# Kernel optimization log

Measured on AMD Instinct MI355X. Metric: run time of the kernel, lower is better.

The kernel has to match this reference:

```python
import jax, jax.numpy as jnp
import numpy as np

B, S, D, H = 4, 2048, 768, 12
DK = D // H


def setup_inputs() -> dict:
    key = jax.random.key(0)
    ks = jax.random.split(key, 12)
    s = 1.0 / np.sqrt(D)
    return {
        "query": jax.random.normal(ks[0], (B, S, D), jnp.float32),
        "key_": jax.random.normal(ks[1], (B, S, D), jnp.float32),
        "value": jax.random.normal(ks[2], (B, S, D), jnp.float32),
        "mask": jax.random.randint(ks[3], (B, S), 0, 2, jnp.int32),
        # nn.Linear weights are (out_features, in_features); y = x @ W.T + b
        "Wq": jax.random.normal(ks[4], (D, D), jnp.float32) * s,
        "bq": jnp.zeros((D,), jnp.float32),
        "Wk": jax.random.normal(ks[5], (D, D), jnp.float32) * s,
        "bk": jnp.zeros((D,), jnp.float32),
        "Wv": jax.random.normal(ks[6], (D, D), jnp.float32) * s,
        "bv": jnp.zeros((D,), jnp.float32),
        "Wo": jax.random.normal(ks[7], (D, D), jnp.float32) * s,
        "bo": jnp.zeros((D,), jnp.float32),
    }


def reference(query, key_, value, mask, Wq, bq, Wk, bk, Wv, bv, Wo, bo):
    b = query.shape[0]
    # QKV projections, split heads: (B, S, D) -> (B, H, S, DK)
    def proj(x, W, bia):
        y = x @ W.T + bia
        return y.reshape(b, -1, H, DK).transpose(0, 2, 1, 3)

    q = proj(query, Wq, bq)
    k = proj(key_, Wk, bk)
    v = proj(value, Wv, bv)

    # Scaled dot-product attention with full [B, H, S, S] score matrix
    scores = jnp.einsum("bhqd,bhkd->bhqk", q, k) / jnp.sqrt(jnp.float32(DK))
    # mask: (B, S) broadcast over heads and query positions; masked_fill(mask==0, -1e9)
    scores = jnp.where(mask[:, None, None, :] == 0, jnp.float32(-1e9), scores)
    attn = jax.nn.softmax(scores, axis=-1)
    x = jnp.einsum("bhqk,bhkd->bhqd", attn, v)  # (B, H, S, DK)

    # merge heads and output projection
    x = x.transpose(0, 2, 1, 3).reshape(b, -1, H * DK)
    return x @ Wo.T + bo
```

## Files before the change

kernel.cpp:

```cpp
#include <hip/hip_runtime.h>
#include <math.h>

#define B_  4
#define S_  2048
#define D_  768
#define H_  12
#define DK_ 64
#define M_  (B_ * S_)
#define NBH_ (B_ * H_)

typedef float f32x4 __attribute__((ext_vector_type(4)));
typedef float f32x16 __attribute__((ext_vector_type(16)));
typedef __bf16 bf16x8 __attribute__((ext_vector_type(8)));
typedef unsigned u32x4v __attribute__((ext_vector_type(4)));

#if __has_builtin(__builtin_amdgcn_exp2f)
#define EXP2(x) __builtin_amdgcn_exp2f(x)
#else
#define EXP2(x) exp2f(x)
#endif

static __device__ __forceinline__ unsigned short f2bf(float f) {
    unsigned u = __builtin_bit_cast(unsigned, f);
    u += 0x7fffu + ((u >> 16) & 1u);
    return (unsigned short)(u >> 16);
}

static __device__ __forceinline__ unsigned cvt_pk_bf16(float lo, float hi) {
    unsigned r;
    asm("v_cvt_pk_bf16_f32 %0, %1, %2" : "=v"(r) : "v"(lo), "v"(hi));
    return r;
}

static __device__ __forceinline__ void gload_lds16(const void* g, void* l) {
    __builtin_amdgcn_global_load_lds(
        (const __attribute__((address_space(1))) void*)g,
        (__attribute__((address_space(3))) void*)l, 16, 0, 0);
}

__global__ __launch_bounds__(256) void cvt_x(
    const float* __restrict__ q, const float* __restrict__ k,
    const float* __restrict__ v,
    unsigned short* __restrict__ q16, unsigned short* __restrict__ k16,
    unsigned short* __restrict__ v16)
{
    const int z = blockIdx.y;
    const float* src = (z == 0) ? q : (z == 1) ? k : v;
    unsigned short* dst = (z == 0) ? q16 : (z == 1) ? k16 : v16;
    const int NG = M_ * 96;
    for (int g = blockIdx.x * 256 + threadIdx.x; g < NG; g += gridDim.x * 256) {
        int r = g / 96, c8 = g - r * 96;
        int kt = c8 >> 2, sl = c8 & 3;
        const float* sp = src + (size_t)r * D_ + kt * 32 + sl * 8;
        float4 a = *(const float4*)sp;
        float4 b = *(const float4*)(sp + 4);
        u32x4v o;
        o.x = cvt_pk_bf16(a.x, a.y); o.y = cvt_pk_bf16(a.z, a.w);
        o.z = cvt_pk_bf16(b.x, b.y); o.w = cvt_pk_bf16(b.z, b.w);
        *(u32x4v*)(dst + (size_t)r * D_ + kt * 32 + ((sl ^ (r & 3)) << 3)) = o;
    }
}

__global__ __launch_bounds__(256) void cvt_w(
    const float* __restrict__ wq, const float* __restrict__ wk,
    const float* __restrict__ wv,
    unsigned short* __restrict__ wq16, unsigned short* __restrict__ wk16,
    unsigned short* __restrict__ wv16)
{
    const int z = blockIdx.y;
    const float* src = (z == 0) ? wq : (z == 1) ? wk : wv;
    unsigned short* dst = (z == 0) ? wq16 : (z == 1) ? wk16 : wv16;
    const int NG = D_ * 96;
    for (int g = blockIdx.x * 256 + threadIdx.x; g < NG; g += gridDim.x * 256) {
        int r = g / 96, c8 = g - r * 96;
        int kt = c8 >> 2, sl = c8 & 3;
        const float* sp = src + (size_t)r * D_ + kt * 32 + sl * 8;
        float4 a = *(const float4*)sp;
        float4 b = *(const float4*)(sp + 4);
        u32x4v o;
        o.x = cvt_pk_bf16(a.x, a.y); o.y = cvt_pk_bf16(a.z, a.w);
        o.z = cvt_pk_bf16(b.x, b.y); o.w = cvt_pk_bf16(b.z, b.w);
        *(u32x4v*)(dst + (size_t)r * D_ + kt * 32 + ((sl ^ (r & 3)) << 3)) = o;
    }
}

static __device__ __forceinline__ void gemm_body_dma(
    const unsigned short* __restrict__ A16, const unsigned short* __restrict__ B16,
    const float* __restrict__ bias, void* __restrict__ outp, const int mode,
    const float oscale)
{
    __shared__ __align__(16) unsigned short As[2][128 * 32];
    __shared__ __align__(16) unsigned short Bs[2][128 * 32];

    const int t  = threadIdx.x;
    const int l  = t & 63;
    const int w  = t >> 6;
    const int lr = l & 15;
    const int lg = l >> 4;
    const int wm = w >> 1;
    const int wn = w & 1;
    const int m0 = blockIdx.x * 128;
    const int n0 = blockIdx.y * 128;

    const unsigned short* adma = A16 + (size_t)(m0 + 32 * w + (l >> 2)) * D_ + (l & 3) * 8;
    const unsigned short* bdma = B16 + (size_t)(n0 + 32 * w + (l >> 2)) * D_ + (l & 3) * 8;

#define GSTAGE(K0, NB) do { \
        gload_lds16(adma + (K0),           &As[NB][(32 * w) * 32]); \
        gload_lds16(adma + (K0) + 16 * D_, &As[NB][(32 * w + 16) * 32]); \
        gload_lds16(bdma + (K0),           &Bs[NB][(32 * w) * 32]); \
        gload_lds16(bdma + (K0) + 16 * D_, &Bs[NB][(32 * w + 16) * 32]); \
    } while (0)

    f32x4 acc[4][4];
#pragma unroll
    for (int mi = 0; mi < 4; mi++)
#pragma unroll
        for (int ni = 0; ni < 4; ni++) acc[mi][ni] = (f32x4){0.f, 0.f, 0.f, 0.f};

    const int fsw = lr & 3;

    GSTAGE(0, 0);
    __syncthreads();

    for (int kt = 0; kt < 24; kt++) {
        const int cur = kt & 1;
        if (kt < 23) {
            if (cur) GSTAGE((kt + 1) * 32, 0);
            else     GSTAGE((kt + 1) * 32, 1);
        }

        bf16x8 af[4], bfr[4];
#pragma unroll
        for (int mi = 0; mi < 4; mi++) {
            int row = wm * 64 + mi * 16 + lr;
            af[mi] = *(const bf16x8*)&As[cur][row * 32 + ((lg ^ fsw) << 3)];
        }
#pragma unroll
        for (int ni = 0; ni < 4; ni++) {
            int row = wn * 64 + ni * 16 + lr;
            bfr[ni] = *(const bf16x8*)&Bs[cur][row * 32 + ((lg ^ fsw) << 3)];
        }
#pragma unroll
        for (int mi = 0; mi < 4; mi++)
#pragma unroll
            for (int ni = 0; ni < 4; ni++)
                acc[mi][ni] = __builtin_amdgcn_mfma_f32_16x16x32_bf16(
                    af[mi], bfr[ni], acc[mi][ni], 0, 0, 0);

        __syncthreads();
    }
#undef GSTAGE

    const int mrow0 = m0 + wm * 64;
    const int ncol0 = n0 + wn * 64;
    if (mode == 2) {
        unsigned short* out = (unsigned short*)outp;
#pragma unroll
        for (int mi = 0; mi < 4; mi++)
#pragma unroll
            for (int ni = 0; ni < 4; ni++) {
                int n = ncol0 + ni * 16 + lr;
                int h = n >> 6, dk = n & 63;
                float bv = bias[n];
                int m = mrow0 + mi * 16 + 4 * lg;
                int b = m >> 11, s = m & (S_ - 1);
                int slotp = ((s >> 3) & 7) ^ (dk & 7);
                int ssw = (s & ~63) | (slotp << 3) | (s & 7);
                uint2 o;
                o.x = cvt_pk_bf16(acc[mi][ni][0] + bv, acc[mi][ni][1] + bv);
                o.y = cvt_pk_bf16(acc[mi][ni][2] + bv, acc[mi][ni][3] + bv);
                *(uint2*)&out[((size_t)(b * H_ + h) * DK_ + dk) * S_ + ssw] = o;
            }
    } else {
        unsigned short* out = (unsigned short*)outp;
#pragma unroll
        for (int mi = 0; mi < 4; mi++)
#pragma unroll
            for (int ni = 0; ni < 4; ni++) {
                int n = ncol0 + ni * 16 + lr;
                int h = n >> 6, dk = n & 63;
                float bv = bias[n];
#pragma unroll
                for (int j = 0; j < 4; j++) {
                    int m = mrow0 + mi * 16 + 4 * lg + j;
                    int b = m >> 11, s = m & (S_ - 1);
                    int dko = (mode == 3)
                        ? ((dk & 7) | ((((dk >> 3) ^ (s & 7))) << 3)) : dk;
                    out[((size_t)(b * H_ + h) * S_ + s) * DK_ + dko] =
                        f2bf((acc[mi][ni][j] + bv) * oscale);
                }
            }
    }
}

__global__ __launch_bounds__(256) void gemm_qkv(
    const unsigned short* __restrict__ q16, const unsigned short* __restrict__ k16,
    const unsigned short* __restrict__ v16,
    const unsigned short* __restrict__ wq16, const unsigned short* __restrict__ wk16,
    const unsigned short* __restrict__ wv16,
    const float* __restrict__ bq, const float* __restrict__ bk,
    const float* __restrict__ bv,
    unsigned short* __restrict__ Qb, unsigned short* __restrict__ Kb,
    unsigned short* __restrict__ VT)
{
    const int z = blockIdx.z;
    const unsigned short* A = (z == 0) ? q16 : (z == 1) ? k16 : v16;
    const unsigned short* W = (z == 0) ? wq16 : (z == 1) ? wk16 : wv16;
    const float* bias = (z == 0) ? bq : (z == 1) ? bk : bv;
    void* out = (z == 0) ? (void*)Qb : (z == 1) ? (void*)Kb : (void*)VT;
    const int mode = (z == 0) ? 0 : (z == 1) ? 3 : 2;
    const float osc = (z == 0) ? 0.18033688011112042f : 1.0f;
    gemm_body_dma(A, W, bias, out, mode, osc);
}

__global__ __launch_bounds__(256) void proj_mfma(
    const float* __restrict__ X, const float* __restrict__ W,
    const float* __restrict__ bias, float* __restrict__ out)
{
    __shared__ __align__(16) unsigned short As[2][128 * 32];
    __shared__ __align__(16) unsigned short Bs[2][128 * 32];

    const int t  = threadIdx.x;
    const int l  = t & 63;
    const int w  = t >> 6;
    const int lr = l & 15;
    const int lg = l >> 4;
    const int wm = w >> 1;
    const int wn = w & 1;
    const int m0 = blockIdx.x * 128;
    const int n0 = blockIdx.y * 128;

    const int v0r = t >> 2,         v0s = t & 3;
    const int v1r = (t + 256) >> 2, v1s = (t + 256) & 3;
    const int off0 = v0r * 32 + ((v0s ^ ((v0r >> 1) & 3)) << 3);
    const int off1 = v1r * 32 + ((v1s ^ ((v1r >> 1) & 3)) << 3);
    const float* xg0 = X + (size_t)(m0 + v0r) * D_ + v0s * 8;
    const float* xg1 = X + (size_t)(m0 + v1r) * D_ + v1s * 8;
    const float* wg0 = W + (size_t)(n0 + v0r) * D_ + v0s * 8;
    const float* wg1 = W + (size_t)(n0 + v1r) * D_ + v1s * 8;

    float4 pxa, pxb, pxc, pxd, pwa, pwb, pwc, pwd;

#define PROJ_LOAD(K0) do { \
        pxa = *(const float4*)(xg0 + (K0)); pxb = *(const float4*)(xg0 + (K0) + 4); \
        pxc = *(const float4*)(xg1 + (K0)); pxd = *(const float4*)(xg1 + (K0) + 4); \
        pwa = *(const float4*)(wg0 + (K0)); pwb = *(const float4*)(wg0 + (K0) + 4); \
        pwc = *(const float4*)(wg1 + (K0)); pwd = *(const float4*)(wg1 + (K0) + 4); \
    } while (0)

#define PROJ_STORE(BUF) do { \
        u32x4v xa_, xb_, wa_, wb_; \
        xa_.x = cvt_pk_bf16(pxa.x, pxa.y); xa_.y = cvt_pk_bf16(pxa.z, pxa.w); \
        xa_.z = cvt_pk_bf16(pxb.x, pxb.y); xa_.w = cvt_pk_bf16(pxb.z, pxb.w); \
        xb_.x = cvt_pk_bf16(pxc.x, pxc.y); xb_.y = cvt_pk_bf16(pxc.z, pxc.w); \
        xb_.z = cvt_pk_bf16(pxd.x, pxd.y); xb_.w = cvt_pk_bf16(pxd.z, pxd.w); \
        wa_.x = cvt_pk_bf16(pwa.x, pwa.y); wa_.y = cvt_pk_bf16(pwa.z, pwa.w); \
        wa_.z = cvt_pk_bf16(pwb.x, pwb.y); wa_.w = cvt_pk_bf16(pwb.z, pwb.w); \
        wb_.x = cvt_pk_bf16(pwc.x, pwc.y); wb_.y = cvt_pk_bf16(pwc.z, pwc.w); \
        wb_.z = cvt_pk_bf16(pwd.x, pwd.y); wb_.w = cvt_pk_bf16(pwd.z, pwd.w); \
        *(u32x4v*)&As[BUF][off0] = xa_; \
        *(u32x4v*)&As[BUF][off1] = xb_; \
        *(u32x4v*)&Bs[BUF][off0] = wa_; \
        *(u32x4v*)&Bs[BUF][off1] = wb_; \
    } while (0)

    f32x4 acc[4][4];
#pragma unroll
    for (int mi = 0; mi < 4; mi++)
#pragma unroll
        for (int ni = 0; ni < 4; ni++) acc[mi][ni] = (f32x4){0.f, 0.f, 0.f, 0.f};

    const int fsw = (lr >> 1) & 3;

    PROJ_LOAD(0);
    PROJ_STORE(0);
    __syncthreads();

    for (int kt = 0; kt < 24; kt++) {
        const int cur = kt & 1;
        const bool more = (kt < 23);

        if (more) PROJ_LOAD((kt + 1) * 32);

        bf16x8 af[4], bfr[4];
#pragma unroll
        for (int mi = 0; mi < 4; mi++) {
            int row = wm * 64 + mi * 16 + lr;
            af[mi] = *(const bf16x8*)&As[cur][row * 32 + ((lg ^ fsw) << 3)];
        }
#pragma unroll
        for (int ni = 0; ni < 4; ni++) {
            int row = wn * 64 + ni * 16 + lr;
            bfr[ni] = *(const bf16x8*)&Bs[cur][row * 32 + ((lg ^ fsw) << 3)];
        }
#pragma unroll
        for (int mi = 0; mi < 4; mi++)
#pragma unroll
            for (int ni = 0; ni < 4; ni++)
                acc[mi][ni] = __builtin_amdgcn_mfma_f32_16x16x32_bf16(
                    af[mi], bfr[ni], acc[mi][ni], 0, 0, 0);

        if (more) PROJ_STORE(cur ^ 1);
        __syncthreads();
    }

#undef PROJ_LOAD
#undef PROJ_STORE

    const int mrow0 = m0 + wm * 64;
    const int ncol0 = n0 + wn * 64;
#pragma unroll
    for (int mi = 0; mi < 4; mi++)
#pragma unroll
        for (int ni = 0; ni < 4; ni++) {
            int n = ncol0 + ni * 16 + lr;
            float bv = bias[n];
#pragma unroll
            for (int j = 0; j < 4; j++) {
                int m = mrow0 + mi * 16 + 4 * lg + j;
                out[(size_t)m * D_ + n] = acc[mi][ni][j] + bv;
            }
        }
}

__global__ __launch_bounds__(256) void attn_mfma(
    const unsigned short* __restrict__ Qb, const unsigned short* __restrict__ Kb,
    const unsigned short* __restrict__ VTb, const int* __restrict__ mask,
    float* __restrict__ O)
{
    __shared__ __align__(16) unsigned short Ks[2][64 * 64];
    __shared__ __align__(16) unsigned short Vs[2][64 * 64];

    const int tid = threadIdx.x;
    const int w  = tid >> 6;
    const int l  = tid & 63;
    const int q  = l & 31;
    const int hl = l >> 5;

    const int bh = blockIdx.x % NBH_;
    const int qt = blockIdx.x / NBH_;
    const int b  = bh / H_;
    const int hh = bh - b * H_;
    const int q0 = qt * 128 + w * 32;

    const unsigned short* qp = Qb + ((size_t)bh * S_ + q0 + q) * DK_;
    bf16x8 qf[4];
#pragma unroll
    for (int c = 0; c < 4; c++)
        qf[c] = *(const bf16x8*)(qp + c * 16 + hl * 8);

    const unsigned qext_sel = (hl == 0) ? 0x00003F80u : 0u;
    const unsigned bias_sel = (hl == 0) ? 0x0000C480u : 0u;
    u32x4v qe; qe.x = qext_sel; qe.y = 0u; qe.z = 0u; qe.w = 0u;
    const bf16x8 qf_ext = __builtin_bit_cast(bf16x8, qe);
    u32x4v on; on.x = on.y = on.z = on.w = 0x3F803F80u;
    const bf16x8 vOnes = __builtin_bit_cast(bf16x8, on);

    f32x16 acc0, acc1, accl;
#pragma unroll
    for (int i = 0; i < 16; i++) { acc0[i] = 0.f; acc1[i] = 0.f; accl[i] = 0.f; }

    const unsigned short* kbase = Kb + (size_t)bh * S_ * DK_;
    const unsigned short* vbase = VTb + (size_t)bh * DK_ * S_;
    const int* mbase = mask + b * S_;

    const unsigned short* kdma = kbase + (16 * w) * DK_ + l * 8;
    const unsigned short* vdma0 = vbase + (size_t)(16 * w + (l >> 3)) * S_ + (l & 7) * 8;
    const unsigned short* vdma1 = vdma0 + (size_t)8 * S_;

#define STAGE_DMA(J0, NB) do { \
        gload_lds16(kdma + (size_t)(J0) * DK_,            &Ks[NB][(16 * w) * 64]); \
        gload_lds16(kdma + (size_t)(J0) * DK_ + 8 * DK_,  &Ks[NB][(16 * w + 8) * 64]); \
        gload_lds16(vdma0 + (J0),                         &Vs[NB][(16 * w) * 64]); \
        gload_lds16(vdma1 + (J0),                         &Vs[NB][(16 * w + 8) * 64]); \
    } while (0)

    STAGE_DMA(0, 0);
    __syncthreads();

    const int fsw = (q & 7) << 3;
    const int kr0o = q * 64;
    const int kr1o = (32 + q) * 64;

    for (int tt = 0; tt < 32; tt++) {
        const int j0  = tt * 64;
        const int cur = tt & 1;

        if (tt < 31) {
            if (cur) STAGE_DMA(j0 + 64, 0); else STAGE_DMA(j0 + 64, 1);
        }

        int mv0 = mbase[j0 + q];
        int mv1 = mbase[j0 + 32 + q];
        u32x4v bw0; bw0.x = (mv0 == 0) ? bias_sel : 0u; bw0.y = 0u; bw0.z = 0u; bw0.w = 0u;
        u32x4v bw1; bw1.x = (mv1 == 0) ? bias_sel : 0u; bw1.y = 0u; bw1.z = 0u; bw1.w = 0u;
        bf16x8 kExt0 = __builtin_bit_cast(bf16x8, bw0);
        bf16x8 kExt1 = __builtin_bit_cast(bf16x8, bw1);

        f32x16 s0, s1;
#pragma unroll
        for (int i = 0; i < 16; i++) { s0[i] = 0.f; s1[i] = 0.f; }
        __builtin_amdgcn_s_setprio(1);
        s0 = __builtin_amdgcn_mfma_f32_32x32x16_bf16(kExt0, qf_ext, s0, 0, 0, 0);
        s1 = __builtin_amdgcn_mfma_f32_32x32x16_bf16(kExt1, qf_ext, s1, 0, 0, 0);
#pragma unroll
        for (int c = 0; c < 4; c++) {
            bf16x8 k0 = *(const bf16x8*)&Ks[cur][kr0o + ((c * 16 + hl * 8) ^ fsw)];
            bf16x8 k1 = *(const bf16x8*)&Ks[cur][kr1o + ((c * 16 + hl * 8) ^ fsw)];
            s0 = __builtin_amdgcn_mfma_f32_32x32x16_bf16(k0, qf[c], s0, 0, 0, 0);
            s1 = __builtin_amdgcn_mfma_f32_32x32x16_bf16(k1, qf[c], s1, 0, 0, 0);
        }
        __builtin_amdgcn_s_setprio(0);

#pragma unroll
        for (int r = 0; r < 16; r++) s0[r] = EXP2(s0[r]);
#pragma unroll
        for (int r = 0; r < 16; r++) s1[r] = EXP2(s1[r]);

#define SVAL(CP, I) (((CP) >> 1) ? s1[I] : s0[I])
        bf16x8 pb[4];
#pragma unroll
        for (int cp = 0; cp < 4; cp++) {
            const int e0 = 8 * (cp & 1);
            unsigned lo0 = cvt_pk_bf16(SVAL(cp, e0 + 0), SVAL(cp, e0 + 1));
            unsigned hi0 = cvt_pk_bf16(SVAL(cp, e0 + 2), SVAL(cp, e0 + 3));
            unsigned lo1 = cvt_pk_bf16(SVAL(cp, e0 + 4), SVAL(cp, e0 + 5));
            unsigned hi1 = cvt_pk_bf16(SVAL(cp, e0 + 6), SVAL(cp, e0 + 7));
            asm("v_permlane32_swap_b32 %0, %1" : "+v"(lo0), "+v"(lo1));
            asm("v_permlane32_swap_b32 %0, %1" : "+v"(hi0), "+v"(hi1));
            u32x4v pw;
            pw.x = lo0; pw.y = hi0; pw.z = lo1; pw.w = hi1;
            pb[cp] = __builtin_bit_cast(bf16x8, pw);
        }
#undef SVAL

        __builtin_amdgcn_s_setprio(1);
#pragma unroll
        for (int cp = 0; cp < 4; cp++) {
            bf16x8 v0 = *(const bf16x8*)&Vs[cur][kr0o + ((cp * 16 + hl * 8) ^ fsw)];
            bf16x8 v1 = *(const bf16x8*)&Vs[cur][kr1o + ((cp * 16 + hl * 8) ^ fsw)];
            acc0 = __builtin_amdgcn_mfma_f32_32x32x16_bf16(v0, pb[cp], acc0, 0, 0, 0);
            acc1 = __builtin_amdgcn_mfma_f32_32x32x16_bf16(v1, pb[cp], acc1, 0, 0, 0);
            accl = __builtin_amdgcn_mfma_f32_32x32x16_bf16(vOnes, pb[cp], accl, 0, 0, 0);
        }
        __builtin_amdgcn_s_setprio(0);

        __syncthreads();
    }
#undef STAGE_DMA

    float inv = 1.f / accl[0];
    float* ob = O + ((size_t)b * S_ + q0 + q) * D_ + hh * DK_;
#pragma unroll
    for (int b2 = 0; b2 < 4; b2++) {
        float4 o;
        o.x = acc0[4 * b2 + 0] * inv;
        o.y = acc0[4 * b2 + 1] * inv;
        o.z = acc0[4 * b2 + 2] * inv;
        o.w = acc0[4 * b2 + 3] * inv;
        *(float4*)(ob + 8 * b2 + 4 * hl) = o;
    }
#pragma unroll
    for (int b2 = 0; b2 < 4; b2++) {
        float4 o;
        o.x = acc1[4 * b2 + 0] * inv;
        o.y = acc1[4 * b2 + 1] * inv;
        o.z = acc1[4 * b2 + 2] * inv;
        o.w = acc1[4 * b2 + 3] * inv;
        *(float4*)(ob + 32 + 8 * b2 + 4 * hl) = o;
    }
}

extern "C" void kernel_launch(void* const* d_in, const int* in_sizes, int n_in,
                              void* d_out, int out_size, void* d_ws, size_t ws_size,
                              hipStream_t stream) {
    (void)in_sizes; (void)n_in; (void)out_size; (void)ws_size;

    const float* query = (const float*)d_in[0];
    const float* key_  = (const float*)d_in[1];
    const float* value = (const float*)d_in[2];
    const int*   mask  = (const int*)d_in[3];
    const float* Wq = (const float*)d_in[4];  const float* bq = (const float*)d_in[5];
    const float* Wk = (const float*)d_in[6];  const float* bk = (const float*)d_in[7];
    const float* Wv = (const float*)d_in[8];  const float* bv = (const float*)d_in[9];
    const float* Wo = (const float*)d_in[10]; const float* bo = (const float*)d_in[11];
    float* out = (float*)d_out;

    const size_t MD = (size_t)M_ * D_;
    const size_t DD = (size_t)D_ * D_;
    unsigned short* q16  = (unsigned short*)d_ws;
    unsigned short* k16  = q16 + MD;
    unsigned short* v16  = k16 + MD;
    unsigned short* Qb   = v16 + MD;
    unsigned short* Kb   = Qb + MD;
    unsigned short* VT   = Kb + MD;
    unsigned short* Wq16 = VT + MD;
    unsigned short* Wk16 = Wq16 + DD;
    unsigned short* Wv16 = Wk16 + DD;
    float* Xb = (float*)q16;

    cvt_x<<<dim3(1024, 3), 256, 0, stream>>>(query, key_, value, q16, k16, v16);
    cvt_w<<<dim3(72, 3), 256, 0, stream>>>(Wq, Wk, Wv, Wq16, Wk16, Wv16);

    gemm_qkv<<<dim3(M_ / 128, D_ / 128, 3), 256, 0, stream>>>(
        q16, k16, v16, Wq16, Wk16, Wv16, bq, bk, bv, Qb, Kb, VT);

    attn_mfma<<<dim3((S_ / 128) * NBH_), 256, 0, stream>>>(Qb, Kb, VT, mask, Xb);

    proj_mfma<<<dim3(M_ / 128, D_ / 128), 256, 0, stream>>>(Xb, Wo, bo, out);
}
```

Before: 199.6 us.

## Emit bf16 swizzled attention output and reuse DMA GEMM for output projection

The attention kernel now writes its output as bf16 in the swizzled layout the DMA GEMM expects, instead of fp32. The output projection is replaced by the shared gemm_body_dma path with a new fp32 store mode, and Wo is converted to bf16 in the weight-conversion kernel. This roughly halves the traffic for the attention output and drops the in-loop fp32-to-bf16 conversion from the old projection kernel. The s_setprio hints around the MFMA blocks in attention are also removed, which may change how wavefronts interleave.

Result: faster. 175.9 us (-11.9%).

```diff
diff --git a/kernel.cpp b/kernel.cpp
--- a/kernel.cpp
+++ b/kernel.cpp
@@ -63,13 +63,13 @@
 
 __global__ __launch_bounds__(256) void cvt_w(
     const float* __restrict__ wq, const float* __restrict__ wk,
-    const float* __restrict__ wv,
+    const float* __restrict__ wv, const float* __restrict__ wo,
     unsigned short* __restrict__ wq16, unsigned short* __restrict__ wk16,
-    unsigned short* __restrict__ wv16)
+    unsigned short* __restrict__ wv16, unsigned short* __restrict__ wo16)
 {
     const int z = blockIdx.y;
-    const float* src = (z == 0) ? wq : (z == 1) ? wk : wv;
-    unsigned short* dst = (z == 0) ? wq16 : (z == 1) ? wk16 : wv16;
+    const float* src = (z == 0) ? wq : (z == 1) ? wk : (z == 2) ? wv : wo;
+    unsigned short* dst = (z == 0) ? wq16 : (z == 1) ? wk16 : (z == 2) ? wv16 : wo16;
     const int NG = D_ * 96;
     for (int g = blockIdx.x * 256 + threadIdx.x; g < NG; g += gridDim.x * 256) {
         int r = g / 96, c8 = g - r * 96;
@@ -154,7 +154,21 @@
 
     const int mrow0 = m0 + wm * 64;
     const int ncol0 = n0 + wn * 64;
-    if (mode == 2) {
+    if (mode == 1) {
+        float* out = (float*)outp;
+#pragma unroll
+        for (int mi = 0; mi < 4; mi++)
+#pragma unroll
+            for (int ni = 0; ni < 4; ni++) {
+                int n = ncol0 + ni * 16 + lr;
+                float bv = bias[n];
+#pragma unroll
+                for (int j = 0; j < 4; j++) {
+                    int m = mrow0 + mi * 16 + 4 * lg + j;
+                    out[(size_t)m * D_ + n] = acc[mi][ni][j] + bv;
+                }
+            }
+    } else if (mode == 2) {
         unsigned short* out = (unsigned short*)outp;
 #pragma unroll
         for (int mi = 0; mi < 4; mi++)
@@ -214,120 +228,17 @@
     gemm_body_dma(A, W, bias, out, mode, osc);
 }
 
-__global__ __launch_bounds__(256) void proj_mfma(
-    const float* __restrict__ X, const float* __restrict__ W,
-    const float* __restrict__ bias, float* __restrict__ out)
-{
-    __shared__ __align__(16) unsigned short As[2][128 * 32];
-    __shared__ __align__(16) unsigned short Bs[2][128 * 32];
-
-    const int t  = threadIdx.x;
-    const int l  = t & 63;
-    const int w  = t >> 6;
-    const int lr = l & 15;
-    const int lg = l >> 4;
-    const int wm = w >> 1;
-    const int wn = w & 1;
-    const int m0 = blockIdx.x * 128;
-    const int n0 = blockIdx.y * 128;
-
-    const int v0r = t >> 2,         v0s = t & 3;
-    const int v1r = (t + 256) >> 2, v1s = (t + 256) & 3;
-    const int off0 = v0r * 32 + ((v0s ^ ((v0r >> 1) & 3)) << 3);
-    const int off1 = v1r * 32 + ((v1s ^ ((v1r >> 1) & 3)) << 3);
-    const float* xg0 = X + (size_t)(m0 + v0r) * D_ + v0s * 8;
-    const float* xg1 = X + (size_t)(m0 + v1r) * D_ + v1s * 8;
-    const float* wg0 = W + (size_t)(n0 + v0r) * D_ + v0s * 8;
-    const float* wg1 = W + (size_t)(n0 + v1r) * D_ + v1s * 8;
-
-    float4 pxa, pxb, pxc, pxd, pwa, pwb, pwc, pwd;
-
-#define PROJ_LOAD(K0) do { \
-        pxa = *(const float4*)(xg0 + (K0)); pxb = *(const float4*)(xg0 + (K0) + 4); \
-        pxc = *(const float4*)(xg1 + (K0)); pxd = *(const float4*)(xg1 + (K0) + 4); \
-        pwa = *(const float4*)(wg0 + (K0)); pwb = *(const float4*)(wg0 + (K0) + 4); \
-        pwc = *(const float4*)(wg1 + (K0)); pwd = *(const float4*)(wg1 + (K0) + 4); \
-    } while (0)
-
-#define PROJ_STORE(BUF) do { \
-        u32x4v xa_, xb_, wa_, wb_; \
-        xa_.x = cvt_pk_bf16(pxa.x, pxa.y); xa_.y = cvt_pk_bf16(pxa.z, pxa.w); \
-        xa_.z = cvt_pk_bf16(pxb.x, pxb.y); xa_.w = cvt_pk_bf16(pxb.z, pxb.w); \
-        xb_.x = cvt_pk_bf16(pxc.x, pxc.y); xb_.y = cvt_pk_bf16(pxc.z, pxc.w); \
-        xb_.z = cvt_pk_bf16(pxd.x, pxd.y); xb_.w = cvt_pk_bf16(pxd.z, pxd.w); \
-        wa_.x = cvt_pk_bf16(pwa.x, pwa.y); wa_.y = cvt_pk_bf16(pwa.z, pwa.w); \
-        wa_.z = cvt_pk_bf16(pwb.x, pwb.y); wa_.w = cvt_pk_bf16(pwb.z, pwb.w); \
-        wb_.x = cvt_pk_bf16(pwc.x, pwc.y); wb_.y = cvt_pk_bf16(pwc.z, pwc.w); \
-        wb_.z = cvt_pk_bf16(pwd.x, pwd.y); wb_.w = cvt_pk_bf16(pwd.z, pwd.w); \
-        *(u32x4v*)&As[BUF][off0] = xa_; \
-        *(u32x4v*)&As[BUF][off1] = xb_; \
-        *(u32x4v*)&Bs[BUF][off0] = wa_; \
-        *(u32x4v*)&Bs[BUF][off1] = wb_; \
-    } while (0)
-
-    f32x4 acc[4][4];
-#pragma unroll
-    for (int mi = 0; mi < 4; mi++)
-#pragma unroll
-        for (int ni = 0; ni < 4; ni++) acc[mi][ni] = (f32x4){0.f, 0.f, 0.f, 0.f};
-
-    const int fsw = (lr >> 1) & 3;
-
-    PROJ_LOAD(0);
-    PROJ_STORE(0);
-    __syncthreads();
-
-    for (int kt = 0; kt < 24; kt++) {
-        const int cur = kt & 1;
-        const bool more = (kt < 23);
-
-        if (more) PROJ_LOAD((kt + 1) * 32);
-
-        bf16x8 af[4], bfr[4];
-#pragma unroll
-        for (int mi = 0; mi < 4; mi++) {
-            int row = wm * 64 + mi * 16 + lr;
-            af[mi] = *(const bf16x8*)&As[cur][row * 32 + ((lg ^ fsw) << 3)];
-        }
-#pragma unroll
-        for (int ni = 0; ni < 4; ni++) {
-            int row = wn * 64 + ni * 16 + lr;
-            bfr[ni] = *(const bf16x8*)&Bs[cur][row * 32 + ((lg ^ fsw) << 3)];
-        }
-#pragma unroll
-        for (int mi = 0; mi < 4; mi++)
-#pragma unroll
-            for (int ni = 0; ni < 4; ni++)
-                acc[mi][ni] = __builtin_amdgcn_mfma_f32_16x16x32_bf16(
-                    af[mi], bfr[ni], acc[mi][ni], 0, 0, 0);
-
-        if (more) PROJ_STORE(cur ^ 1);
-        __syncthreads();
-    }
-
-#undef PROJ_LOAD
-#undef PROJ_STORE
-
-    const int mrow0 = m0 + wm * 64;
-    const int ncol0 = n0 + wn * 64;
-#pragma unroll
-    for (int mi = 0; mi < 4; mi++)
-#pragma unroll
-        for (int ni = 0; ni < 4; ni++) {
-            int n = ncol0 + ni * 16 + lr;
-            float bv = bias[n];
-#pragma unroll
-            for (int j = 0; j < 4; j++) {
-                int m = mrow0 + mi * 16 + 4 * lg + j;
-                out[(size_t)m * D_ + n] = acc[mi][ni][j] + bv;
-            }
-        }
+__global__ __launch_bounds__(256) void gemm_o(
+    const unsigned short* __restrict__ X16, const unsigned short* __restrict__ wo16,
+    const float* __restrict__ bo, float* __restrict__ out)
+{
+    gemm_body_dma(X16, wo16, bo, (void*)out, 1, 1.0f);
 }
 
 __global__ __launch_bounds__(256) void attn_mfma(
     const unsigned short* __restrict__ Qb, const unsigned short* __restrict__ Kb,
     const unsigned short* __restrict__ VTb, const int* __restrict__ mask,
-    float* __restrict__ O)
+    unsigned short* __restrict__ Xb16)
 {
     __shared__ __align__(16) unsigned short Ks[2][64 * 64];
     __shared__ __align__(16) unsigned short Vs[2][64 * 64];
@@ -401,7 +312,6 @@
         f32x16 s0, s1;
 #pragma unroll
         for (int i = 0; i < 16; i++) { s0[i] = 0.f; s1[i] = 0.f; }
-        __builtin_amdgcn_s_setprio(1);
         s0 = __builtin_amdgcn_mfma_f32_32x32x16_bf16(kExt0, qf_ext, s0, 0, 0, 0);
         s1 = __builtin_amdgcn_mfma_f32_32x32x16_bf16(kExt1, qf_ext, s1, 0, 0, 0);
 #pragma unroll
@@ -411,7 +321,6 @@
             s0 = __builtin_amdgcn_mfma_f32_32x32x16_bf16(k0, qf[c], s0, 0, 0, 0);
             s1 = __builtin_amdgcn_mfma_f32_32x32x16_bf16(k1, qf[c], s1, 0, 0, 0);
         }
-        __builtin_amdgcn_s_setprio(0);
 
 #pragma unroll
         for (int r = 0; r < 16; r++) s0[r] = EXP2(s0[r]);
@@ -435,7 +344,6 @@
         }
 #undef SVAL
 
-        __builtin_amdgcn_s_setprio(1);
 #pragma unroll
         for (int cp = 0; cp < 4; cp++) {
             bf16x8 v0 = *(const bf16x8*)&Vs[cur][kr0o + ((cp * 16 + hl * 8) ^ fsw)];
@@ -444,31 +352,24 @@
             acc1 = __builtin_amdgcn_mfma_f32_32x32x16_bf16(v1, pb[cp], acc1, 0, 0, 0);
             accl = __builtin_amdgcn_mfma_f32_32x32x16_bf16(vOnes, pb[cp], accl, 0, 0, 0);
         }
-        __builtin_amdgcn_s_setprio(0);
 
         __syncthreads();
     }
 #undef STAGE_DMA
 
     float inv = 1.f / accl[0];
-    float* ob = O + ((size_t)b * S_ + q0 + q) * D_ + hh * DK_;
+    unsigned short* ob = Xb16 + ((size_t)b * S_ + q0 + q) * D_ + hh * DK_;
+    const int rsw = q & 3;
 #pragma unroll
     for (int b2 = 0; b2 < 4; b2++) {
-        float4 o;
-        o.x = acc0[4 * b2 + 0] * inv;
-        o.y = acc0[4 * b2 + 1] * inv;
-        o.z = acc0[4 * b2 + 2] * inv;
-        o.w = acc0[4 * b2 + 3] * inv;
-        *(float4*)(ob + 8 * b2 + 4 * hl) = o;
-    }
-#pragma unroll
-    for (int b2 = 0; b2 < 4; b2++) {
-        float4 o;
-        o.x = acc1[4 * b2 + 0] * inv;
-        o.y = acc1[4 * b2 + 1] * inv;
-        o.z = acc1[4 * b2 + 2] * inv;
-        o.w = acc1[4 * b2 + 3] * inv;
-        *(float4*)(ob + 32 + 8 * b2 + 4 * hl) = o;
+        uint2 o0;
+        o0.x = cvt_pk_bf16(acc0[4 * b2 + 0] * inv, acc0[4 * b2 + 1] * inv);
+        o0.y = cvt_pk_bf16(acc0[4 * b2 + 2] * inv, acc0[4 * b2 + 3] * inv);
+        *(uint2*)(ob + (((b2 ^ rsw) << 3) + 4 * hl)) = o0;
+        uint2 o1;
+        o1.x = cvt_pk_bf16(acc1[4 * b2 + 0] * inv, acc1[4 * b2 + 1] * inv);
+        o1.y = cvt_pk_bf16(acc1[4 * b2 + 2] * inv, acc1[4 * b2 + 3] * inv);
+        *(uint2*)(ob + 32 + (((b2 ^ rsw) << 3) + 4 * hl)) = o1;
     }
 }
 
@@ -495,18 +396,19 @@
     unsigned short* Qb   = v16 + MD;
     unsigned short* Kb   = Qb + MD;
     unsigned short* VT   = Kb + MD;
-    unsigned short* Wq16 = VT + MD;
+    unsigned short* Xb16 = VT + MD;
+    unsigned short* Wq16 = Xb16 + MD;
     unsigned short* Wk16 = Wq16 + DD;
     unsigned short* Wv16 = Wk16 + DD;
-    float* Xb = (float*)q16;
+    unsigned short* Wo16 = Wv16 + DD;
 
     cvt_x<<<dim3(1024, 3), 256, 0, stream>>>(query, key_, value, q16, k16, v16);
-    cvt_w<<<dim3(72, 3), 256, 0, stream>>>(Wq, Wk, Wv, Wq16, Wk16, Wv16);
+    cvt_w<<<dim3(72, 4), 256, 0, stream>>>(Wq, Wk, Wv, Wo, Wq16, Wk16, Wv16, Wo16);
 
     gemm_qkv<<<dim3(M_ / 128, D_ / 128, 3), 256, 0, stream>>>(
         q16, k16, v16, Wq16, Wk16, Wv16, bq, bk, bv, Qb, Kb, VT);
 
-    attn_mfma<<<dim3((S_ / 128) * NBH_), 256, 0, stream>>>(Qb, Kb, VT, mask, Xb);
-
-    proj_mfma<<<dim3(M_ / 128, D_ / 128), 256, 0, stream>>>(Xb, Wo, bo, out);
-}
+    attn_mfma<<<dim3((S_ / 128) * NBH_), 256, 0, stream>>>(Qb, Kb, VT, mask, Xb16);
+
+    gemm_o<<<dim3(M_ / 128, D_ / 128), 256, 0, stream>>>(Xb16, Wo16, bo, out);
+}
```
